# Performance work log

Hardware: AMD Instinct MI355X
Metric: run time of the kernel (lower is better)

Reference implementation:

```python
import jax, jax.numpy as jnp
import numpy as np

H = 24        # attn.heads (Flux)
ENC = 512     # encoder (text) token count, hard-coded in the source via emb[:512]
EPS = 1e-6    # RMSNorm eps


def _rms(x, w):
    # RMSNorm over head_dim (Flux norm_q / norm_k)
    return x * jax.lax.rsqrt(jnp.mean(x * x, axis=-1, keepdims=True) + EPS) * w


def _rope(x, cos, sin):
    # diffusers apply_rotary_emb, use_real=True, unbind_dim=-1
    xr = x.reshape(x.shape[:-1] + (-1, 2))
    rot = jnp.stack([-xr[..., 1], xr[..., 0]], axis=-1).reshape(x.shape)
    return x * cos + rot * sin


def setup_inputs() -> dict:
    key = jax.random.key(0)
    ks = jax.random.split(key, 26)
    B, F, D = 2, 1024, 3072
    hd = D // H
    S = ENC + F
    lin = lambda k: 0.02 * jax.random.normal(k, (D, D), jnp.float32)
    bias = lambda k: 0.02 * jax.random.normal(k, (D,), jnp.float32)
    nw = lambda k: 1.0 + 0.02 * jax.random.normal(k, (hd,), jnp.float32)
    return {
        'hidden_states': jax.random.normal(ks[0], (B, F, D), jnp.float32),
        'encoder_hidden_states': jax.random.normal(ks[1], (B, ENC, D), jnp.float32),
        'rot_cos': jax.random.uniform(ks[2], (S, hd), jnp.float32, minval=-1.0, maxval=1.0),
        'rot_sin': jax.random.uniform(ks[3], (S, hd), jnp.float32, minval=-1.0, maxval=1.0),
        'wq': lin(ks[4]), 'bq': bias(ks[5]),
        'wk': lin(ks[6]), 'bk': bias(ks[7]),
        'wv': lin(ks[8]), 'bv': bias(ks[9]),
        'waq': lin(ks[10]), 'baq': bias(ks[11]),
        'wak': lin(ks[12]), 'bak': bias(ks[13]),
        'wav': lin(ks[14]), 'bav': bias(ks[15]),
        'wo': lin(ks[16]), 'bo': bias(ks[17]),
        'wao': lin(ks[18]), 'bao': bias(ks[19]),
        'nq': nw(ks[20]), 'nk': nw(ks[21]),
        'naq': nw(ks[22]), 'nak': nw(ks[23]),
    }


def reference(hidden_states, encoder_hidden_states, rot_cos, rot_sin,
              wq, bq, wk, bk, wv, bv, waq, baq, wak, bak, wav, bav,
              wo, bo, wao, bao, nq, nk, naq, nak):
    B, F, D = hidden_states.shape
    hd = D // H

    def proj(x, w, b):
        y = x @ w.T + b
        return y.reshape(x.shape[0], -1, H, hd).transpose(0, 2, 1, 3)  # [B,H,S,hd]

    q = _rms(proj(hidden_states, wq, bq), nq)   # [B,H,F,hd]
    k = _rms(proj(hidden_states, wk, bk), nk)
    v = proj(hidden_states, wv, bv)

    # cross-batch mixing: 'b h f d -> 1 h (b f) d' then repeat over batch
    k = jnp.broadcast_to(k.transpose(1, 0, 2, 3).reshape(1, H, B * F, hd), (B, H, B * F, hd))
    v = jnp.broadcast_to(v.transpose(1, 0, 2, 3).reshape(1, H, B * F, hd), (B, H, B * F, hd))

    # key rotary: encoder part once, image part repeated num_components times
    cos_k = jnp.concatenate([rot_cos[:ENC]] + [rot_cos[ENC:]] * B, axis=0)
    sin_k = jnp.concatenate([rot_sin[:ENC]] + [rot_sin[ENC:]] * B, axis=0)

    eq = _rms(proj(encoder_hidden_states, waq, baq), naq)  # [B,H,ENC,hd]
    ek = _rms(proj(encoder_hidden_states, wak, bak), nak)
    ev = proj(encoder_hidden_states, wav, bav)

    q = jnp.concatenate([eq, q], axis=2)  # [B,H,ENC+F,hd]
    k = jnp.concatenate([ek, k], axis=2)  # [B,H,ENC+B*F,hd]
    v = jnp.concatenate([ev, v], axis=2)

    q = _rope(q, rot_cos, rot_sin)
    k = _rope(k, cos_k, sin_k)

    scale = hd ** -0.5
    attn = jax.nn.softmax(jnp.einsum('bhqd,bhkd->bhqk', q, k) * scale, axis=-1)
    out = jnp.einsum('bhqk,bhkd->bhqd', attn, v)
    out = out.transpose(0, 2, 1, 3).reshape(B, -1, D)  # [B,ENC+F,D]

    enc_out = out[:, :ENC] @ wao.T + bao
    hs_out = out[:, ENC:] @ wo.T + bo
    return (hs_out, enc_out)
```

## Files before the change

### kernel.cpp

```cpp
#include <hip/hip_runtime.h>

typedef __attribute__((ext_vector_type(8))) short bf16x8;
typedef __attribute__((ext_vector_type(8))) unsigned short u16x8;
typedef __attribute__((ext_vector_type(4))) unsigned short u16x4;
typedef __attribute__((ext_vector_type(4))) float f32x4;
typedef __attribute__((ext_vector_type(2))) unsigned uint2v;

#define DEV static __device__ __forceinline__

DEV unsigned short f2bf(float f){
  unsigned u = __float_as_uint(f);
  u += 0x7fff + ((u>>16)&1);
  return (unsigned short)(u>>16);
}
DEV float bf2f(unsigned short b){ return __uint_as_float(((unsigned)b)<<16); }
DEV unsigned cvtpk(float lo, float hi){
  unsigned r;
  asm("v_cvt_pk_bf16_f32 %0, %1, %2" : "=v"(r) : "v"(lo), "v"(hi));
  return r;
}

DEV void gll16(const void* g, void* l){
  __builtin_amdgcn_global_load_lds((__attribute__((address_space(1))) unsigned*)(void*)g,
                                   (__attribute__((address_space(3))) unsigned*)l, 16, 0, 0);
}

__global__ void k_cast(const float* __restrict__ x, unsigned short* __restrict__ y, int n4){
  int i = blockIdx.x*256 + threadIdx.x;
  if (i >= n4) return;
  f32x4 v = ((const f32x4*)x)[i];
  u16x4 o = { f2bf(v.x), f2bf(v.y), f2bf(v.z), f2bf(v.w) };
  ((u16x4*)y)[i] = o;
}

__global__ void k_castW(const float* __restrict__ s0, const float* __restrict__ s1,
                        const float* __restrict__ s2, const float* __restrict__ s3,
                        const float* __restrict__ s4, const float* __restrict__ s5,
                        unsigned short* __restrict__ y){
  unsigned i = blockIdx.x*256 + threadIdx.x;
  unsigned seg = i / 2359296u;
  unsigned off = i - seg*2359296u;
  const float* s = seg==0?s0: seg==1?s1: seg==2?s2: seg==3?s3: seg==4?s4: s5;
  f32x4 v = ((const f32x4*)s)[off];
  u16x4 o = { f2bf(v.x), f2bf(v.y), f2bf(v.z), f2bf(v.w) };
  ((u16x4*)y)[i] = o;
}

__global__ void k_castW2(const float* __restrict__ s0, const float* __restrict__ s1,
                         unsigned short* __restrict__ y){
  unsigned i = blockIdx.x*256 + threadIdx.x;
  unsigned seg = i / 2359296u;
  unsigned off = i - seg*2359296u;
  const float* s = seg==0?s0:s1;
  f32x4 v = ((const f32x4*)s)[off];
  u16x4 o = { f2bf(v.x), f2bf(v.y), f2bf(v.z), f2bf(v.w) };
  ((u16x4*)y)[i] = o;
}

__global__ __launch_bounds__(256) void k_gemmP(
    const unsigned short* __restrict__ X, const unsigned short* __restrict__ W,
    const float* __restrict__ b0, const float* __restrict__ b1, const float* __restrict__ b2,
    const float* __restrict__ nqw, const float* __restrict__ nkw,
    const float* __restrict__ cs, const float* __restrict__ sn,
    unsigned short* __restrict__ Qd, unsigned short* __restrict__ Kd,
    unsigned short* __restrict__ Vd,
    int is_img)
{
  const int K = 3072;
  __shared__ unsigned short SH[17408];
  unsigned short (*As)[4096] = (unsigned short(*)[4096])SH;
  unsigned short (*Bs)[4096] = (unsigned short(*)[4096])(SH + 8192);
  const int t = threadIdx.x, w = t>>6, l = t&63;
  const int li = l&15, g = l>>4;
  const int by = blockIdx.y, bx = blockIdx.x;
  const int sec = by>=48 ? 2 : (by>=24 ? 1 : 0);
  const int hd = by - sec*24;
  const int Cl = hd*128;
  const int R = bx*128;
  const unsigned short* Wp = W + (long)sec*9437184 + (long)Cl*K;
  const float* bias = (sec==0)?b0:(sec==1)?b1:b2;
  const int wr = w>>1, wc = w&1;
  f32x4 acc[4][4] = {};

  auto stage = [&](int buf, int kt){
    const int k0 = kt*32;
    #pragma unroll
    for (int c=0;c<2;c++){
      int row = c*64 + (t>>2);
      int scol = ((t&3)<<3) ^ ((row&3)<<3);
      gll16(X + (long)(R+row)*K + k0 + scol, &As[buf][c*2048 + w*512]);
      gll16(Wp + (long)row*K + k0 + scol, &Bs[buf][c*2048 + w*512]);
    }
  };

  stage(0,0);
  int buf = 0;
  for (int kt=0; kt<96; kt++){
    __syncthreads();
    if (kt+1 < 96) stage(buf^1, kt+1);
    bf16x8 a[4], b[4];
    #pragma unroll
    for (int m=0;m<4;m++){
      int ar = wr*64 + m*16 + li;
      int ac = (g<<3) ^ ((ar&3)<<3);
      a[m] = *(const bf16x8*)&As[buf][ar*32 + ac];
      int br = wc*64 + m*16 + li;
      int bc2 = (g<<3) ^ ((br&3)<<3);
      b[m] = *(const bf16x8*)&Bs[buf][br*32 + bc2];
    }
    #pragma unroll
    for (int m=0;m<4;m++)
      #pragma unroll
      for (int n=0;n<4;n++)
        acc[m][n] = __builtin_amdgcn_mfma_f32_16x16x32_bf16(a[m], b[n], acc[m][n], 0,0,0);
    buf ^= 1;
  }

  float bias_n[4];
  #pragma unroll
  for (int n=0;n<4;n++) bias_n[n] = bias[Cl + wc*64 + n*16 + li];

  if (sec == 2){
    __syncthreads();
    unsigned short* SHT = SH;
    #pragma unroll
    for (int m=0;m<4;m++){
      int tok_l = wr*64 + m*16 + (g<<2);
      #pragma unroll
      for (int n=0;n<4;n++){
        int col_l = wc*64 + n*16 + li;
        u16x4 v4 = { f2bf(acc[m][n][0]+bias_n[n]), f2bf(acc[m][n][1]+bias_n[n]),
                     f2bf(acc[m][n][2]+bias_n[n]), f2bf(acc[m][n][3]+bias_n[n]) };
        *(u16x4*)&SHT[col_l*136 + tok_l] = v4;
      }
    }
    __syncthreads();
    int d = t>>1, half = t&1;
    int tok0 = R + half*64;
    long base;
    if (is_img) base = ((long)hd*128 + d)*2048 + tok0;
    else { int b_ = tok0>>9, s_ = tok0&511; base = ((long)(b_*24+hd)*128 + d)*512 + s_; }
    #pragma unroll
    for (int k2=0;k2<8;k2++)
      *(u16x8*)(Vd + base + k2*8) = *(const u16x8*)&SHT[d*136 + half*64 + k2*8];
    return;
  }

  float part[4][4];
  #pragma unroll
  for (int m=0;m<4;m++)
    #pragma unroll
    for (int r=0;r<4;r++){
      float s_ = 0.f;
      #pragma unroll
      for (int n=0;n<4;n++){ float v = acc[m][n][r] + bias_n[n]; s_ += v*v; }
      part[m][r] = s_;
    }
  #pragma unroll
  for (int m=0;m<4;m++)
    #pragma unroll
    for (int r=0;r<4;r++){
      part[m][r] += __shfl_xor(part[m][r], 1);
      part[m][r] += __shfl_xor(part[m][r], 2);
      part[m][r] += __shfl_xor(part[m][r], 4);
      part[m][r] += __shfl_xor(part[m][r], 8);
    }
  __syncthreads();
  float* rs = (float*)SH;
  if (li == 0){
    #pragma unroll
    for (int m=0;m<4;m++)
      #pragma unroll
      for (int r=0;r<4;r++)
        rs[(wc*2+wr)*64 + m*16 + g*4 + r] = part[m][r];
  }
  __syncthreads();
  float fac[4][4];
  #pragma unroll
  for (int m=0;m<4;m++)
    #pragma unroll
    for (int r=0;r<4;r++){
      int idx = m*16 + g*4 + r;
      float tot = rs[(0*2+wr)*64 + idx] + rs[(1*2+wr)*64 + idx];
      fac[m][r] = rsqrtf(tot*(1.0f/128.0f) + 1e-6f);
    }

  const float* nw = (sec==0) ? nqw : nkw;
  const float qs = (sec==0) ? (float)(0.08838834764831845 * 1.4426950408889634) : 1.0f;
  float nw_n[4];
  #pragma unroll
  for (int n=0;n<4;n++) nw_n[n] = nw[wc*64 + n*16 + li];

  #pragma unroll
  for (int m=0;m<4;m++){
    #pragma unroll
    for (int r=0;r<4;r++){
      int row_l = wr*64 + m*16 + g*4 + r;
      int t_row = R + row_l;
      int b_, s_, p_;
      if (is_img){ b_ = t_row>>10; s_ = t_row&1023; p_ = 512+s_; }
      else       { b_ = t_row>>9;  s_ = t_row&511;  p_ = s_; }
      long didx;
      if (sec==0) didx = (long)(b_*24+hd)*1536 + (is_img ? 512+s_ : s_);
      else        didx = is_img ? ((long)hd*2048 + t_row) : ((long)(b_*24+hd)*512 + s_);
      const float* crow = cs + (long)p_*128;
      const float* srow = sn + (long)p_*128;
      unsigned short* drow = ((sec==0)?Qd:Kd) + didx*128;
      #pragma unroll
      for (int n=0;n<4;n++){
        int cl = wc*64 + n*16 + li;
        float x = (acc[m][n][r] + bias_n[n]) * fac[m][r] * nw_n[n];
        float xo = __shfl_xor(x, 1);
        float o_ = x*crow[cl] + ((l&1) ? xo*srow[cl] : -xo*srow[cl]);
        drow[cl] = f2bf(o_*qs);
      }
    }
  }
}

__global__ __launch_bounds__(256) void k_gemmO(
    const unsigned short* __restrict__ X, const unsigned short* __restrict__ Wf,
    float* __restrict__ out, const float* __restrict__ bo, const float* __restrict__ bao)
{
  const int K = 3072;
  __shared__ unsigned short As[2][4096];
  __shared__ unsigned short Bs[2][4096];
  const int t = threadIdx.x, w = t>>6, l = t&63;
  const int bx = blockIdx.x, by = blockIdx.y;
  const bool enc = bx >= 16;
  const unsigned short* Wp = Wf + (enc ? 9437184 : 0);
  const float* bias = enc ? bao : bo;
  const int R = bx*128, C = by*128;
  long xbase, obase;
  if (!enc){ xbase = (long)(R>>10)*1536 + 512 + (R&1023); obase = (long)R*3072; }
  else { int Rp = R-2048; xbase = (long)(Rp>>9)*1536 + (Rp&511); obase = 6291456 + (long)Rp*3072; }
  const int wr = w>>1, wc = w&1;
  f32x4 acc[4][4] = {};

  auto stage = [&](int buf, int kt){
    const int k0 = kt*32;
    #pragma unroll
    for (int c=0;c<2;c++){
      int row = c*64 + (t>>2);
      int scol = ((t&3)<<3) ^ ((row&3)<<3);
      gll16(X + (xbase+row)*K + k0 + scol, &As[buf][c*2048 + w*512]);
      gll16(Wp + (long)(C+row)*K + k0 + scol, &Bs[buf][c*2048 + w*512]);
    }
  };

  stage(0,0);
  int buf = 0;
  for (int kt=0; kt<96; kt++){
    __syncthreads();
    if (kt+1 < 96) stage(buf^1, kt+1);
    bf16x8 a[4], b[4];
    #pragma unroll
    for (int m=0;m<4;m++){
      int ar = wr*64 + m*16 + (l&15);
      int ac = ((l>>4)<<3) ^ ((ar&3)<<3);
      a[m] = *(const bf16x8*)&As[buf][ar*32 + ac];
      int br = wc*64 + m*16 + (l&15);
      int bc2 = ((l>>4)<<3) ^ ((br&3)<<3);
      b[m] = *(const bf16x8*)&Bs[buf][br*32 + bc2];
    }
    #pragma unroll
    for (int m=0;m<4;m++)
      #pragma unroll
      for (int n=0;n<4;n++)
        acc[m][n] = __builtin_amdgcn_mfma_f32_16x16x32_bf16(a[m], b[n], acc[m][n], 0,0,0);
    buf ^= 1;
  }

  #pragma unroll
  for (int m=0;m<4;m++){
    int rl = wr*64 + m*16 + ((l>>4)<<2);
    #pragma unroll
    for (int n=0;n<4;n++){
      int col = C + wc*64 + n*16 + (l&15);
      float bvv = bias[col];
      #pragma unroll
      for (int r=0;r<4;r++)
        out[obase + (long)(rl+r)*3072 + col] = acc[m][n][r] + bvv;
    }
  }
}

__global__ __launch_bounds__(256) void k_attn(
    const unsigned short* __restrict__ Q,
    const unsigned short* __restrict__ Ke, const unsigned short* __restrict__ Ki,
    const unsigned short* __restrict__ Ve, const unsigned short* __restrict__ Vi,
    unsigned short* __restrict__ AO)
{
  __shared__ unsigned short Ks[8192];
  __shared__ unsigned short Vs[8192];
  __shared__ unsigned short Ps[4][1408];
  const int t = threadIdx.x, w = t>>6, l = t&63;
  const int h = blockIdx.y, b = blockIdx.z;
  const int bh = b*24 + h;
  const int q0 = blockIdx.x*64 + w*16;
  const int g = l>>4;

  auto stageK = [&](int jt){
    const unsigned short* ksrc = (jt < 8) ? Ke + ((long)bh*512 + jt*64)*128
                                          : Ki + ((long)h*2048 + (jt-8)*64)*128;
    #pragma unroll
    for (int c=0;c<4;c++){
      int row = c*16 + (t>>4);
      int col = ((t&15)<<3) ^ ((row&7)<<3);
      gll16(ksrc + row*128 + col, &Ks[c*2048 + w*512]);
    }
  };
  auto stageV = [&](int jt){
    const unsigned short* vsrc; long vstr;
    if (jt < 8){ vsrc = Ve + (long)bh*65536 + jt*64; vstr = 512; }
    else { vsrc = Vi + (long)h*262144 + (jt-8)*64; vstr = 2048; }
    #pragma unroll
    for (int c=0;c<4;c++){
      int row = c*32 + (t>>3);
      int col = ((t&7)<<3) ^ ((row&7)<<3);
      gll16(vsrc + (long)row*vstr + col, &Vs[c*2048 + w*512]);
    }
  };

  bf16x8 qf[4];
  {
    const unsigned short* qp = Q + ((long)bh*1536 + q0 + (l&15))*128 + (g<<3);
    #pragma unroll
    for (int kc=0;kc<4;kc++) qf[kc] = *(const bf16x8*)(qp + kc*32);
  }
  f32x4 o[8] = {};
  float mx = -1e30f;
  float ls = 0.f;

  stageK(0);
  for (int jt=0; jt<40; jt++){
    __syncthreads();
    stageV(jt);

    f32x4 sf[4];
    __builtin_amdgcn_s_setprio(1);
    #pragma unroll
    for (int ct=0;ct<4;ct++){
      f32x4 s = {};
      #pragma unroll
      for (int kc=0;kc<4;kc++){
        int krow = ct*16 + (l&15);
        int kcol = (kc*32 + (g<<3)) ^ ((krow&7)<<3);
        bf16x8 kb = *(const bf16x8*)&Ks[krow*128 + kcol];
        s = __builtin_amdgcn_mfma_f32_16x16x32_bf16(kb, qf[kc], s, 0,0,0);
      }
      sf[ct] = s;
    }
    __builtin_amdgcn_s_setprio(0);

    float pm = sf[0][0];
    #pragma unroll
    for (int ct=0;ct<4;ct++)
      #pragma unroll
      for (int r=0;r<4;r++) pm = fmaxf(pm, sf[ct][r]);
    if (!__all(pm <= mx + 8.0f)){
      float tmax = pm;
      tmax = fmaxf(tmax, __shfl_xor(tmax, 16));
      tmax = fmaxf(tmax, __shfl_xor(tmax, 32));
      float mn = fmaxf(mx, tmax);
      float al = exp2f(mx - mn);
      mx = mn;
      ls *= al;
      #pragma unroll
      for (int r=0;r<4;r++){
        float alo = __shfl(al, (l&48) | ((g<<2)+r));
        #pragma unroll
        for (int f=0;f<8;f++) o[f][r] *= alo;
      }
    }
    #pragma unroll
    for (int ct=0;ct<4;ct++){
      float p0 = exp2f(sf[ct][0]-mx), p1 = exp2f(sf[ct][1]-mx);
      float p2 = exp2f(sf[ct][2]-mx), p3 = exp2f(sf[ct][3]-mx);
      ls += (p0+p1)+(p2+p3);
      uint2v pk = { cvtpk(p0,p1), cvtpk(p2,p3) };
      *(uint2v*)&Ps[w][(l&15)*88 + ct*16 + (g<<2)] = pk;
    }
    __syncthreads();

    if (jt+1 < 40) stageK(jt+1);

    bf16x8 pa[2];
    #pragma unroll
    for (int kc=0;kc<2;kc++)
      pa[kc] = *(const bf16x8*)&Ps[w][(l&15)*88 + kc*32 + (g<<3)];
    __builtin_amdgcn_s_setprio(1);
    #pragma unroll
    for (int f=0;f<8;f++){
      #pragma unroll
      for (int kc=0;kc<2;kc++){
        int vrow = f*16 + (l&15);
        int vcol = (kc*32 + (g<<3)) ^ ((vrow&7)<<3);
        bf16x8 vb = *(const bf16x8*)&Vs[vrow*64 + vcol];
        o[f] = __builtin_amdgcn_mfma_f32_16x16x32_bf16(pa[kc], vb, o[f], 0,0,0);
      }
    }
    __builtin_amdgcn_s_setprio(0);
  }

  ls += __shfl_xor(ls, 16);
  ls += __shfl_xor(ls, 32);
  #pragma unroll
  for (int r=0;r<4;r++){
    float lso = __shfl(ls, (l&48) | ((g<<2)+r));
    float inv = 1.0f/lso;
    int qrow = q0 + (g<<2) + r;
    #pragma unroll
    for (int f=0;f<8;f++){
      AO[((long)b*1536 + qrow)*3072 + h*128 + f*16 + (l&15)] = f2bf(o[f][r]*inv);
    }
  }
}

extern "C" void kernel_launch(void* const* d_in, const int* in_sizes, int n_in,
                              void* d_out, int out_size, void* d_ws, size_t ws_size,
                              hipStream_t stream)
{
  const float* hs  = (const float*)d_in[0];
  const float* ehs = (const float*)d_in[1];
  const float* rc  = (const float*)d_in[2];
  const float* rs_ = (const float*)d_in[3];
  const float* wq = (const float*)d_in[4];  const float* bq = (const float*)d_in[5];
  const float* wk = (const float*)d_in[6];  const float* bk = (const float*)d_in[7];
  const float* wv = (const float*)d_in[8];  const float* bv = (const float*)d_in[9];
  const float* waq= (const float*)d_in[10]; const float* baq= (const float*)d_in[11];
  const float* wak= (const float*)d_in[12]; const float* bak= (const float*)d_in[13];
  const float* wav= (const float*)d_in[14]; const float* bav= (const float*)d_in[15];
  const float* wo = (const float*)d_in[16]; const float* bo = (const float*)d_in[17];
  const float* wao= (const float*)d_in[18]; const float* bao= (const float*)d_in[19];
  const float* nq = (const float*)d_in[20]; const float* nk = (const float*)d_in[21];
  const float* naq= (const float*)d_in[22]; const float* nak= (const float*)d_in[23];

  char* p = (char*)d_ws;
  auto alloc = [&](size_t bytes){ char* r = p; p += bytes; return r; };

  if (ws_size >= (size_t)188743680){
    unsigned short* Xh = (unsigned short*)alloc(12582912);
    unsigned short* Xe = (unsigned short*)alloc(6291456);
    unsigned short* Wb = (unsigned short*)alloc(113246208);
    unsigned short* Qb = (unsigned short*)alloc(18874368);
    unsigned short* Ke = (unsigned short*)alloc(6291456);
    unsigned short* Ki = (unsigned short*)alloc(12582912);
    unsigned short* Ve = (unsigned short*)alloc(6291456);
    unsigned short* Vi = (unsigned short*)alloc(12582912);
    unsigned short* AO = Xh;

    k_cast<<<6144,256,0,stream>>>(hs, Xh, 1572864);
    k_cast<<<3072,256,0,stream>>>(ehs, Xe, 786432);
    k_castW<<<55296,256,0,stream>>>(wq, wk, wv, waq, wak, wav, Wb);

    k_gemmP<<<dim3(16,72),256,0,stream>>>(Xh, Wb, bq, bk, bv,
                                          nq, nk, rc, rs_, Qb, Ki, Vi, 1);
    k_gemmP<<<dim3(8,72),256,0,stream>>>(Xe, Wb + 28311552, baq, bak, bav,
                                         naq, nak, rc, rs_, Qb, Ke, Ve, 0);

    k_attn<<<dim3(24,24,2),256,0,stream>>>(Qb, Ke, Ki, Ve, Vi, AO);

    k_castW2<<<18432,256,0,stream>>>(wo, wao, Wb);
    k_gemmO<<<dim3(24,24),256,0,stream>>>(AO, Wb, (float*)d_out, bo, bao);
  } else {
    unsigned short* Xh = (unsigned short*)alloc(12582912);
    unsigned short* Xe = (unsigned short*)alloc(6291456);
    unsigned short* Wb = (unsigned short*)alloc(56623104);
    unsigned short* Qb = (unsigned short*)alloc(18874368);
    unsigned short* Ke = (unsigned short*)alloc(6291456);
    unsigned short* Ki = (unsigned short*)alloc(12582912);
    unsigned short* Ve = (unsigned short*)alloc(6291456);
    unsigned short* Vi = (unsigned short*)alloc(12582912);
    unsigned short* AO = Xh;

    k_cast<<<6144,256,0,stream>>>(hs, Xh, 1572864);
    k_cast<<<3072,256,0,stream>>>(ehs, Xe, 786432);

    k_cast<<<9216,256,0,stream>>>(wq, Wb, 2359296);
    k_cast<<<9216,256,0,stream>>>(wk, Wb + 9437184, 2359296);
    k_cast<<<9216,256,0,stream>>>(wv, Wb + 18874368, 2359296);
    k_gemmP<<<dim3(16,72),256,0,stream>>>(Xh, Wb, bq, bk, bv,
                                          nq, nk, rc, rs_, Qb, Ki, Vi, 1);

    k_cast<<<9216,256,0,stream>>>(waq, Wb, 2359296);
    k_cast<<<9216,256,0,stream>>>(wak, Wb + 9437184, 2359296);
    k_cast<<<9216,256,0,stream>>>(wav, Wb + 18874368, 2359296);
    k_gemmP<<<dim3(8,72),256,0,stream>>>(Xe, Wb, baq, bak, bav,
                                         naq, nak, rc, rs_, Qb, Ke, Ve, 0);

    k_attn<<<dim3(24,24,2),256,0,stream>>>(Qb, Ke, Ki, Ve, Vi, AO);

    k_castW2<<<18432,256,0,stream>>>(wo, wao, Wb);
    k_gemmO<<<dim3(24,24),256,0,stream>>>(AO, Wb, (float*)d_out, bo, bao);
  }
}
```

Before: 694.8 us.

## Shrink projection GEMM LDS, refine swizzle, split V transpose into two passes

Sets the projection GEMM's shared buffer to exactly the double-buffered tile size (32KB) and adds a min-blocks launch bound so more workgroups can be resident per CU. The V-section epilogue transpose now runs in two passes over 64-column halves, so it fits in the smaller buffer. The LDS swizzle in both GEMMs gains an extra XOR on row bit 3 to reduce bank conflicts on the fragment reads. Costs: an extra barrier pass in the V epilogue, and possible register pressure or spills from the occupancy hint.

```diff
diff --git a/kernel.cpp b/kernel.cpp
--- a/kernel.cpp
+++ b/kernel.cpp
@@ -57,7 +57,7 @@
   ((u16x4*)y)[i] = o;
 }
 
-__global__ __launch_bounds__(256) void k_gemmP(
+__global__ __launch_bounds__(256, 5) void k_gemmP(
     const unsigned short* __restrict__ X, const unsigned short* __restrict__ W,
     const float* __restrict__ b0, const float* __restrict__ b1, const float* __restrict__ b2,
     const float* __restrict__ nqw, const float* __restrict__ nkw,
@@ -67,7 +67,7 @@
     int is_img)
 {
   const int K = 3072;
-  __shared__ unsigned short SH[17408];
+  __shared__ unsigned short SH[16384];
   unsigned short (*As)[4096] = (unsigned short(*)[4096])SH;
   unsigned short (*Bs)[4096] = (unsigned short(*)[4096])(SH + 8192);
   const int t = threadIdx.x, w = t>>6, l = t&63;
@@ -87,7 +87,7 @@
     #pragma unroll
     for (int c=0;c<2;c++){
       int row = c*64 + (t>>2);
-      int scol = ((t&3)<<3) ^ ((row&3)<<3);
+      int scol = ((t&3)<<3) ^ ((row&3)<<3) ^ (((row>>3)&1)<<4);
       gll16(X + (long)(R+row)*K + k0 + scol, &As[buf][c*2048 + w*512]);
       gll16(Wp + (long)row*K + k0 + scol, &Bs[buf][c*2048 + w*512]);
     }
@@ -102,10 +102,10 @@
     #pragma unroll
     for (int m=0;m<4;m++){
       int ar = wr*64 + m*16 + li;
-      int ac = (g<<3) ^ ((ar&3)<<3);
+      int ac = (g<<3) ^ ((ar&3)<<3) ^ (((ar>>3)&1)<<4);
       a[m] = *(const bf16x8*)&As[buf][ar*32 + ac];
       int br = wc*64 + m*16 + li;
-      int bc2 = (g<<3) ^ ((br&3)<<3);
+      int bc2 = (g<<3) ^ ((br&3)<<3) ^ (((br>>3)&1)<<4);
       b[m] = *(const bf16x8*)&Bs[buf][br*32 + bc2];
     }
     #pragma unroll
@@ -121,28 +121,34 @@
   for (int n=0;n<4;n++) bias_n[n] = bias[Cl + wc*64 + n*16 + li];
 
   if (sec == 2){
-    __syncthreads();
     unsigned short* SHT = SH;
     #pragma unroll
-    for (int m=0;m<4;m++){
-      int tok_l = wr*64 + m*16 + (g<<2);
-      #pragma unroll
-      for (int n=0;n<4;n++){
-        int col_l = wc*64 + n*16 + li;
-        u16x4 v4 = { f2bf(acc[m][n][0]+bias_n[n]), f2bf(acc[m][n][1]+bias_n[n]),
-                     f2bf(acc[m][n][2]+bias_n[n]), f2bf(acc[m][n][3]+bias_n[n]) };
-        *(u16x4*)&SHT[col_l*136 + tok_l] = v4;
+    for (int pass=0; pass<2; pass++){
+      __syncthreads();
+      if (wc == pass){
+        #pragma unroll
+        for (int m=0;m<4;m++){
+          int tok_l = wr*64 + m*16 + (g<<2);
+          #pragma unroll
+          for (int n=0;n<4;n++){
+            int col_loc = n*16 + li;
+            u16x4 v4 = { f2bf(acc[m][n][0]+bias_n[n]), f2bf(acc[m][n][1]+bias_n[n]),
+                         f2bf(acc[m][n][2]+bias_n[n]), f2bf(acc[m][n][3]+bias_n[n]) };
+            *(u16x4*)&SHT[col_loc*136 + tok_l] = v4;
+          }
+        }
       }
-    }
-    __syncthreads();
-    int d = t>>1, half = t&1;
-    int tok0 = R + half*64;
-    long base;
-    if (is_img) base = ((long)hd*128 + d)*2048 + tok0;
-    else { int b_ = tok0>>9, s_ = tok0&511; base = ((long)(b_*24+hd)*128 + d)*512 + s_; }
-    #pragma unroll
-    for (int k2=0;k2<8;k2++)
-      *(u16x8*)(Vd + base + k2*8) = *(const u16x8*)&SHT[d*136 + half*64 + k2*8];
+      __syncthreads();
+      int d_loc = t>>2, qtr = t&3;
+      int d = pass*64 + d_loc;
+      int tok0 = R + qtr*32;
+      long base;
+      if (is_img) base = ((long)hd*128 + d)*2048 + tok0;
+      else { int b_ = tok0>>9, s_ = tok0&511; base = ((long)(b_*24+hd)*128 + d)*512 + s_; }
+      #pragma unroll
+      for (int k2=0;k2<4;k2++)
+        *(u16x8*)(Vd + base + k2*8) = *(const u16x8*)&SHT[d_loc*136 + qtr*32 + k2*8];
+    }
     return;
   }
 
@@ -242,7 +248,7 @@
     #pragma unroll
     for (int c=0;c<2;c++){
       int row = c*64 + (t>>2);
-      int scol = ((t&3)<<3) ^ ((row&3)<<3);
+      int scol = ((t&3)<<3) ^ ((row&3)<<3) ^ (((row>>3)&1)<<4);
       gll16(X + (xbase+row)*K + k0 + scol, &As[buf][c*2048 + w*512]);
       gll16(Wp + (long)(C+row)*K + k0 + scol, &Bs[buf][c*2048 + w*512]);
     }
@@ -257,10 +263,10 @@
     #pragma unroll
     for (int m=0;m<4;m++){
       int ar = wr*64 + m*16 + (l&15);
-      int ac = ((l>>4)<<3) ^ ((ar&3)<<3);
+      int ac = ((l>>4)<<3) ^ ((ar&3)<<3) ^ (((ar>>3)&1)<<4);
       a[m] = *(const bf16x8*)&As[buf][ar*32 + ac];
       int br = wc*64 + m*16 + (l&15);
-      int bc2 = ((l>>4)<<3) ^ ((br&3)<<3);
+      int bc2 = ((l>>4)<<3) ^ ((br&3)<<3) ^ (((br>>3)&1)<<4);
       b[m] = *(const bf16x8*)&Bs[buf][br*32 + bc2];
     }
     #pragma unroll
```

Measured after the change: 713.9 us. +2.7%, slower.
